# Performance work log

Hardware: AMD Instinct MI355X
Metric: run time of the kernel (lower is better)

## Reference

```python
import jax, jax.numpy as jnp
import numpy as np

B, T, D = 8, 2048, 512
S = 4                 # n_slots
SLOT_DIM = D          # cfg.slot_dim defaults to d_model
SE = 8                # state_embed_dim
GH = 64               # gate_hidden
EMA = 0.99
SIGMA_FLOOR = 1e-3
OPEN2CLOSING, CLOSING2LOCKED, UNLOCK = 0.1, 0.03, 0.25
GAINS = jnp.array([1.0, 0.5, 0.1], dtype=jnp.float32)  # OPEN, CLOSING, LOCKED


def _glorot(k, shape, fi, fo):
    b = (6.0 / (fi + fo)) ** 0.5
    return jax.random.uniform(k, shape, jnp.float32, -b, b)


def setup_inputs() -> dict:
    key = jax.random.key(0)
    ks = jax.random.split(key, 8)
    gate_in = D + 1 + SE  # [h, z, state_embed]
    return {
        'h_seq': jax.random.normal(ks[0], (B, T, D), jnp.float32),
        'pred_W': _glorot(ks[1], (S, D, D), D, D),
        'pred_b': jnp.zeros((S, D), jnp.float32),
        'gate_W1': _glorot(ks[2], (S, gate_in, GH), gate_in, GH),
        'gate_b1': jnp.zeros((S, GH), jnp.float32),
        'gate_W2': _glorot(ks[3], (S, GH, 1), GH, 1),
        'gate_b2': jnp.zeros((S, 1), jnp.float32),
        'write_W': _glorot(ks[4], (S, D, SLOT_DIM), D, SLOT_DIM),
        'write_b': jnp.zeros((S, SLOT_DIM), jnp.float32),
        'w0': jnp.zeros((S, SLOT_DIM), jnp.float32),
        'state_embed': jax.random.normal(ks[5], (3, SE), jnp.float32),
    }


def reference(h_seq, pred_W, pred_b, gate_W1, gate_b1, gate_W2, gate_b2,
              write_W, write_b, w0, state_embed):
    Bb, Tt, Dd = h_seq.shape
    h_det = jax.lax.stop_gradient(h_seq)
    # per-slot next-step predictions (input detached, as in torch): (B,T,S,D)
    preds = jnp.einsum('btd,sdo->btso', h_det, pred_W) + pred_b
    # prediction emitted at t-1 targets h_t
    pred_prev = jnp.concatenate([jnp.zeros_like(preds[:, :1]), preds[:, :-1]], axis=1)
    valid = jnp.arange(Tt) > 0  # no surprise signal at t=0

    m0 = jnp.broadcast_to(w0, (Bb, S, SLOT_DIM)).astype(h_seq.dtype)
    carry0 = (m0,
              jnp.zeros((S,), jnp.float32),       # mu
              jnp.ones((S,), jnp.float32),        # sigma
              jnp.full((S,), 0.5, jnp.float32),   # gate_ema
              jnp.zeros((S,), jnp.int32))         # slot_state

    def step(carry, xs):
        m, mu, sigma, gate_ema, state = carry
        h_t, p_prev, ok = xs  # (B,D), (B,S,D), scalar bool
        # prediction-error surprise per slot
        err = jnp.sqrt(jnp.sum((p_prev - h_t[:, None, :]) ** 2, axis=-1) + 1e-8)  # (B,S)
        err = jnp.where(ok, err, 0.0)
        z = (err - mu) / jnp.maximum(sigma, SIGMA_FLOOR)  # (B,S)
        # gate MLP over [h, z, state_embed]
        se = state_embed[state]  # (S,SE)
        gin = jnp.concatenate([
            jnp.broadcast_to(h_t[:, None, :], (Bb, S, Dd)),
            z[..., None],
            jnp.broadcast_to(se[None], (Bb, S, SE))], axis=-1)
        hid = jax.nn.relu(jnp.einsum('bsi,sih->bsh', gin, gate_W1) + gate_b1)
        g = jax.nn.sigmoid(jnp.einsum('bsh,sho->bso', hid, gate_W2) + gate_b2)[..., 0]  # (B,S)
        # state-dependent write gain (OPEN/CLOSING/LOCKED)
        g_eff = g * GAINS[state]
        w_enc = jnp.einsum('bd,sdo->bso', h_t, write_W) + write_b
        m = (1.0 - g_eff[..., None]) * m + g_eff[..., None] * w_enc
        read = m.reshape(Bb, S * SLOT_DIM)
        # homeostatic bookkeeping (buffers: non-differentiable, EMA)
        err_s = jax.lax.stop_gradient(err)
        mu_n = jnp.where(ok, EMA * mu + (1 - EMA) * err_s.mean(0), mu)
        sigma_n = jnp.where(ok, EMA * sigma + (1 - EMA) * jnp.abs(err_s - mu).mean(0), sigma)
        gate_ema_n = EMA * gate_ema + (1 - EMA) * jax.lax.stop_gradient(g).mean(0)
        # state machine transitions on gate EMA
        st = jnp.where((state == 0) & (gate_ema_n < OPEN2CLOSING), 1, state)
        st = jnp.where((state == 1) & (gate_ema_n < CLOSING2LOCKED), 2,
             jnp.where((state == 1) & (gate_ema_n > UNLOCK), 0, st))
        st = jnp.where((state == 2) & (gate_ema_n > UNLOCK), 0, st)
        return (m, mu_n, sigma_n, gate_ema_n, st), read

    xs = (jnp.swapaxes(h_seq, 0, 1), jnp.swapaxes(pred_prev, 0, 1), valid)
    _, reads = jax.lax.scan(step, carry0, xs)
    return jnp.swapaxes(reads, 0, 1)  # (B,T,S*SLOT_DIM)
```

## Files before the change

### kernel.cpp

```cpp
#include <hip/hip_runtime.h>
#include <hip/hip_bf16.h>

#define Bb 8
#define Tt 2048
#define Dd 512
#define Ss 4
#define GHh 64
#define NCHUNK 64
#define CH 32

typedef __hip_bfloat16 bf16;
typedef short bf16x8 __attribute__((ext_vector_type(8)));
typedef short bf16x4 __attribute__((ext_vector_type(4)));
typedef float f32x4 __attribute__((ext_vector_type(4)));
__device__ __forceinline__ float b2f(bf16 x){ return __bfloat162float(x); }
__device__ __forceinline__ float b2fs(short x){ bf16 t; __builtin_memcpy(&t,&x,2); return __bfloat162float(t); }

#define GLOAD_LDS16(g, l) \
  __builtin_amdgcn_global_load_lds((const __attribute__((address_space(1))) unsigned int*)(const void*)(g), \
                                   (__attribute__((address_space(3))) unsigned int*)(l), 16, 0, 0)

__global__ __launch_bounds__(256) void k0a_cvt(const float* __restrict__ h, bf16* __restrict__ hb){
  int i = (blockIdx.x*256 + threadIdx.x)*4;
  float4 v = *reinterpret_cast<const float4*>(&h[i]);
  hb[i+0] = __float2bfloat16(v.x);
  hb[i+1] = __float2bfloat16(v.y);
  hb[i+2] = __float2bfloat16(v.z);
  hb[i+3] = __float2bfloat16(v.w);
}

__global__ __launch_bounds__(256) void k0b_pack(const float* __restrict__ predW,
    const float* __restrict__ writeW, const float* __restrict__ gateW1, bf16* __restrict__ Wt){
  __shared__ float tile[32][33];
  int k0 = blockIdx.x*32, n0 = blockIdx.y*32;
  int tx = threadIdx.x & 31, ty = threadIdx.x >> 5;
  #pragma unroll
  for (int p = 0; p < 4; ++p) {
    int kk = ty + p*8;
    int n = n0 + tx, k = k0 + kk;
    float v;
    if (n < 2048)      { int s=n>>9, o=n&511;              v = predW[((size_t)s*512+k)*512+o]; }
    else if (n < 4096) { int n2=n-2048; int s=n2>>9,o=n2&511; v = writeW[((size_t)s*512+k)*512+o]; }
    else               { int n2=n-4096; int s=n2>>6,hh=n2&63; v = gateW1[((size_t)s*521+k)*64+hh]; }
    tile[kk][tx] = v;
  }
  __syncthreads();
  #pragma unroll
  for (int p = 0; p < 4; ++p) {
    int nn = ty + p*8;
    Wt[(size_t)(n0+nn)*512 + k0 + tx] = __float2bfloat16(tile[tx][nn]);
  }
}

__global__ __launch_bounds__(256) void k1_mfma(
    const bf16* __restrict__ hb, const bf16* __restrict__ Wt,
    const float* __restrict__ h, const float* __restrict__ predb, const float* __restrict__ writeb,
    bf16* __restrict__ wenc, float* __restrict__ hg, float* __restrict__ errsq)
{
  __shared__ bf16 As[2][128*64];
  __shared__ bf16 Bs[2][128*64];
  const int tid = threadIdx.x;
  const int w = tid >> 6, lane = tid & 63;
  const int bid = blockIdx.x;
  const int work = (bid & 7) * 544 + (bid >> 3);
  const int n0   = (work % 34) * 128;
  const int row0 = (work / 34) * 128;
  const int wm = w & 1, wn = w >> 1;
  const int mrow = lane & 15, kq = lane >> 4;

  f32x4 acc[4][4];
  #pragma unroll
  for (int i=0;i<4;++i)
    #pragma unroll
    for (int j=0;j<4;++j) acc[i][j] = (f32x4){0.f,0.f,0.f,0.f};

  const int srow  = lane >> 3;
  const int sslot = (lane & 7) ^ srow;
  const bf16* gaBase = hb + (size_t)(row0 + w*32 + srow)*512 + sslot*8;
  const bf16* gbBase = Wt + (size_t)(n0  + w*32 + srow)*512 + sslot*8;

  auto STAGE = [&](int buf, int kstep){
    const bf16* ga = gaBase + kstep*64;
    const bf16* gb = gbBase + kstep*64;
    bf16* lA = &As[buf][(w*32)*64];
    bf16* lB = &Bs[buf][(w*32)*64];
    #pragma unroll
    for (int i=0;i<4;++i) {
      GLOAD_LDS16(ga + (size_t)i*8*512, lA + i*8*64);
      GLOAD_LDS16(gb + (size_t)i*8*512, lB + i*8*64);
    }
  };

  auto COMPUTE = [&](int buf){
    #pragma unroll
    for (int kk=0; kk<2; ++kk) {
      bf16x8 af[4], bfr[4];
      #pragma unroll
      for (int mi=0;mi<4;++mi) {
        int r = wm*64 + mi*16 + mrow;
        af[mi] = *reinterpret_cast<const bf16x8*>(&As[buf][r*64 + (((kk*4+kq) ^ (r&7))<<3)]);
      }
      #pragma unroll
      for (int ni=0;ni<4;++ni) {
        int r = wn*64 + ni*16 + mrow;
        bfr[ni] = *reinterpret_cast<const bf16x8*>(&Bs[buf][r*64 + (((kk*4+kq) ^ (r&7))<<3)]);
      }
      #pragma unroll
      for (int mi=0;mi<4;++mi)
        #pragma unroll
        for (int ni=0;ni<4;++ni)
          acc[mi][ni] = __builtin_amdgcn_mfma_f32_16x16x32_bf16(af[mi], bfr[ni], acc[mi][ni], 0, 0, 0);
    }
  };

  STAGE(0, 0);
  __syncthreads();
  #pragma unroll
  for (int t = 0; t < 8; ++t) {
    if (t < 7) STAGE((t+1)&1, t+1);
    COMPUTE(t&1);
    __syncthreads();
  }

  if (n0 < 2048) {
    const int s = n0 >> 9;
    #pragma unroll
    for (int mi=0;mi<4;++mi) {
      #pragma unroll
      for (int reg=0;reg<4;++reg) {
        int r = row0 + wm*64 + mi*16 + kq*4 + reg;
        float sum = 0.f;
        if ((r & 2047) != 2047) {
          #pragma unroll
          for (int ni=0;ni<4;++ni) {
            int o = (n0 & 511) + wn*64 + ni*16 + mrow;
            float P = acc[mi][ni][reg] + predb[s*512 + o];
            float d = P - h[(size_t)(r+1)*512 + o];
            sum = fmaf(d, d, sum);
          }
        }
        #pragma unroll
        for (int off=1; off<16; off<<=1) sum += __shfl_xor(sum, off);
        if (mrow == 0 && (r & 2047) != 2047)
          atomicAdd(&errsq[(size_t)(r+1)*4 + s], sum);
      }
    }
  } else if (n0 < 4096) {
    #pragma unroll
    for (int mi=0;mi<4;++mi)
      #pragma unroll
      for (int ni=0;ni<4;++ni) {
        int n2 = n0 - 2048 + wn*64 + ni*16 + mrow;
        int s = n2 >> 9, o = n2 & 511;
        float wb = writeb[s*512 + o];
        #pragma unroll
        for (int reg=0;reg<4;++reg) {
          int r = row0 + wm*64 + mi*16 + kq*4 + reg;
          wenc[((size_t)r*4 + s)*512 + o] = __float2bfloat16(acc[mi][ni][reg] + wb);
        }
      }
  } else {
    #pragma unroll
    for (int mi=0;mi<4;++mi)
      #pragma unroll
      for (int ni=0;ni<4;++ni) {
        int n2 = n0 - 4096 + wn*64 + ni*16 + mrow;
        int s = n2 >> 6, hh = n2 & 63;
        #pragma unroll
        for (int reg=0;reg<4;++reg) {
          int r = row0 + wm*64 + mi*16 + kq*4 + reg;
          hg[((size_t)r*4 + s)*64 + hh] = acc[mi][ni][reg];
        }
      }
  }
}

__global__ void k2ab(const float* __restrict__ errsq, float* __restrict__ err, float* __restrict__ em){
  int i = blockIdx.x*256 + threadIdx.x;
  int t = i >> 2;
  float sum = 0.f;
  #pragma unroll
  for (int b=0;b<8;++b){
    float e = (t > 0) ? sqrtf(errsq[b*8192 + i] + 1e-8f) : 0.f;
    err[b*8192 + i] = e;
    sum += e;
  }
  em[i] = sum * 0.125f;
}

__global__ __launch_bounds__(256) void k2c_scan(const float* __restrict__ in, float* __restrict__ outv, float init){
  __shared__ float s_in[8192];
  __shared__ float sA[256], sB[256], s_entry[256];
  for (int i = threadIdx.x; i < 8192; i += 256) s_in[i] = in[i];
  __syncthreads();
  const int c = threadIdx.x >> 2, s = threadIdx.x & 3;
  float A = 1.f, B = 0.f;
  #pragma unroll 8
  for (int i = 0; i < 32; ++i) {
    int t = c*32 + i;
    if (t >= 1) { A *= 0.99f; B = fmaf(0.99f, B, 0.01f * s_in[t*4 + s]); }
  }
  sA[threadIdx.x] = A; sB[threadIdx.x] = B;
  __syncthreads();
  if (threadIdx.x < 4) {
    int ss = threadIdx.x;
    float v = init;
    for (int cc = 0; cc < 64; ++cc) {
      s_entry[cc*4 + ss] = v;
      v = fmaf(sA[cc*4 + ss], v, sB[cc*4 + ss]);
    }
  }
  __syncthreads();
  float v = s_entry[threadIdx.x];
  #pragma unroll 8
  for (int i = 0; i < 32; ++i) {
    int t = c*32 + i;
    outv[t*4 + s] = v;
    if (t >= 1) v = fmaf(0.99f, v, 0.01f * s_in[t*4 + s]);
  }
}

__global__ void k2d_sd(const float* __restrict__ err, const float* __restrict__ MU, float* __restrict__ sd){
  int i = blockIdx.x*256 + threadIdx.x;
  float mu = MU[i];
  float sum = 0.f;
  #pragma unroll
  for (int b=0;b<8;++b) sum += fabsf(err[b*8192 + i] - mu);
  sd[i] = sum * 0.125f;
}

__global__ void k2e_base(const float* __restrict__ gateW1, const float* __restrict__ semb,
                         const float* __restrict__ gateb1, float* __restrict__ base1){
  int i = blockIdx.x*256 + threadIdx.x;
  if (i < 768) {
    int hh = i & 63, k = (i >> 6) % 3, s = i / 192;
    float acc = gateb1[s*64 + hh];
    #pragma unroll
    for (int e = 0; e < 8; ++e)
      acc = fmaf(semb[k*8+e], gateW1[((size_t)s*521 + 513 + e)*64 + hh], acc);
    base1[i] = acc;
  }
}

__global__ void k3_gall(const float* __restrict__ hg, const float* __restrict__ err,
    const float* __restrict__ MU, const float* __restrict__ SIG,
    const float* __restrict__ gateW1, const float* __restrict__ base1,
    const float* __restrict__ gateW2, const float* __restrict__ gateb2,
    float* __restrict__ g_all)
{
  int i = blockIdx.x*256 + threadIdx.x;
  int k = i % 3;
  int bts = i / 3;
  int s = bts & 3;
  int t = (bts >> 2) & 2047;
  float e = err[bts];
  float z = (e - MU[t*4+s]) / fmaxf(SIG[t*4+s], 1e-3f);
  const float4* hgp  = reinterpret_cast<const float4*>(&hg[(size_t)bts*64]);
  const float4* b1p  = reinterpret_cast<const float4*>(&base1[(s*3 + k)*64]);
  const float4* w1zp = reinterpret_cast<const float4*>(&gateW1[((size_t)s*521 + 512)*64]);
  const float4* w2p  = reinterpret_cast<const float4*>(&gateW2[s*64]);
  float logit = 0.f;
  #pragma unroll
  for (int hq = 0; hq < 16; ++hq) {
    float4 hv = hgp[hq], bv = b1p[hq], wz = w1zp[hq], w2 = w2p[hq];
    logit = fmaf(fmaxf(fmaf(z, wz.x, hv.x) + bv.x, 0.f), w2.x, logit);
    logit = fmaf(fmaxf(fmaf(z, wz.y, hv.y) + bv.y, 0.f), w2.y, logit);
    logit = fmaf(fmaxf(fmaf(z, wz.z, hv.z) + bv.z, 0.f), w2.z, logit);
    logit = fmaf(fmaxf(fmaf(z, wz.w, hv.w) + bv.w, 0.f), w2.w, logit);
  }
  logit += gateb2[s];
  g_all[i] = 1.f/(1.f + expf(-logit));
}

__global__ void k3b_gm(const float* __restrict__ g_all, float* __restrict__ gm){
  int i = blockIdx.x*256 + threadIdx.x;
  float sum = 0.f;
  #pragma unroll
  for (int b=0;b<8;++b) sum += g_all[((size_t)b*8192 + i/3)*3 + (i%3)];
  gm[i] = sum * 0.125f;
}

__global__ __launch_bounds__(256) void k4_scan(const float* __restrict__ gm, int* __restrict__ states){
  __shared__ float s_gm[2][6144];
  for (int i = threadIdx.x; i < 6144; i += 256) s_gm[0][i] = gm[i];
  __syncthreads();
  float ema = 0.5f; int st = 0;
  for (int c = 0; c < 4; ++c) {
    if (c < 3)
      for (int i = threadIdx.x; i < 6144; i += 256) s_gm[(c+1)&1][i] = gm[(c+1)*6144 + i];
    if (threadIdx.x < 4) {
      int s = threadIdx.x;
      const float* gp = &s_gm[c&1][s*3];
      int* sp = &states[c*2048 + s];
      #pragma unroll 8
      for (int tt = 0; tt < 512; ++tt) {
        sp[tt*4] = st;
        float g0 = gp[tt*12+0], g1 = gp[tt*12+1], g2 = gp[tt*12+2];
        float base = 0.99f * ema;
        float e0 = fmaf(0.01f, g0, base);
        float e1 = fmaf(0.01f, g1, base);
        float e2 = fmaf(0.01f, g2, base);
        ema = (st == 0) ? e0 : ((st == 1) ? e1 : e2);
        int n0 = (ema < 0.1f) ? 1 : 0;
        int n1 = (ema < 0.03f) ? 2 : ((ema > 0.25f) ? 0 : 1);
        int n2 = (ema > 0.25f) ? 0 : 2;
        st = (st == 0) ? n0 : ((st == 1) ? n1 : n2);
      }
    }
    __syncthreads();
  }
}

__global__ void k5_a(const float* __restrict__ g_all, const int* __restrict__ states, float* __restrict__ a){
  int i = blockIdx.x*256 + threadIdx.x;
  int ts = i & 8191;
  int st = states[ts];
  float gain = (st == 0) ? 1.f : ((st == 1) ? 0.5f : 0.1f);
  a[i] = g_all[(size_t)i*3 + st] * gain;
}

__global__ __launch_bounds__(64) void k6_pass1(const float* __restrict__ a, const bf16* __restrict__ wenc,
      float* __restrict__ q, float* __restrict__ Pc){
  int c = blockIdx.x, s = blockIdx.y, b = blockIdx.z;
  int d0 = threadIdx.x * 4;
  __shared__ float s_a[CH];
  if (threadIdx.x < CH) s_a[threadIdx.x] = a[(size_t)(b*2048 + c*CH + threadIdx.x)*4 + s];
  __syncthreads();
  float qv[8];
  #pragma unroll
  for (int j=0;j<8;++j) qv[j] = 0.f;
  float p = 1.f;
  const bf16* wp = &wenc[((size_t)(b*2048 + c*CH)*4 + s)*512];
  #pragma unroll 4
  for (int i = 0; i < CH; ++i) {
    float av = s_a[i];
    float om = 1.f - av;
    bf16x4 w1 = *reinterpret_cast<const bf16x4*>(wp + (size_t)i*2048 + d0);
    bf16x4 w2 = *reinterpret_cast<const bf16x4*>(wp + (size_t)i*2048 + 256 + d0);
    #pragma unroll
    for (int j=0;j<4;++j) qv[j]   = fmaf(om, qv[j],   av*b2fs(w1[j]));
    #pragma unroll
    for (int j=0;j<4;++j) qv[4+j] = fmaf(om, qv[4+j], av*b2fs(w2[j]));
    p *= om;
  }
  float* qp = &q[((size_t)(b*4+s)*NCHUNK + c)*512];
  *reinterpret_cast<float4*>(qp + d0)       = make_float4(qv[0],qv[1],qv[2],qv[3]);
  *reinterpret_cast<float4*>(qp + 256 + d0) = make_float4(qv[4],qv[5],qv[6],qv[7]);
  if (threadIdx.x == 0) Pc[(b*4+s)*NCHUNK + c] = p;
}

__global__ __launch_bounds__(128) void k7_bound(const float* __restrict__ q, const float* __restrict__ Pc,
      const float* __restrict__ w0, float* __restrict__ m_start){
  int s = blockIdx.x, b = blockIdx.y, d4 = threadIdx.x * 4;
  float4 m = *reinterpret_cast<const float4*>(&w0[s*512 + d4]);
  for (int c = 0; c < NCHUNK; ++c) {
    *reinterpret_cast<float4*>(&m_start[((size_t)(b*4+s)*NCHUNK + c)*512 + d4]) = m;
    float pc = Pc[(b*4+s)*NCHUNK + c];
    float4 qv = *reinterpret_cast<const float4*>(&q[((size_t)(b*4+s)*NCHUNK + c)*512 + d4]);
    m.x = fmaf(pc, m.x, qv.x);
    m.y = fmaf(pc, m.y, qv.y);
    m.z = fmaf(pc, m.z, qv.z);
    m.w = fmaf(pc, m.w, qv.w);
  }
}

__global__ __launch_bounds__(64) void k8_pass2(const float* __restrict__ a, const bf16* __restrict__ wenc,
      const float* __restrict__ m_start, float* __restrict__ out){
  int c = blockIdx.x, s = blockIdx.y, b = blockIdx.z;
  int d0 = threadIdx.x * 4;
  __shared__ float s_a[CH];
  if (threadIdx.x < CH) s_a[threadIdx.x] = a[(size_t)(b*2048 + c*CH + threadIdx.x)*4 + s];
  __syncthreads();
  const float* msp = &m_start[((size_t)(b*4+s)*NCHUNK + c)*512];
  float4 m1 = *reinterpret_cast<const float4*>(msp + d0);
  float4 m2 = *reinterpret_cast<const float4*>(msp + 256 + d0);
  const bf16* wp = &wenc[((size_t)(b*2048 + c*CH)*4 + s)*512];
  float* op = &out[((size_t)(b*2048 + c*CH))*2048 + s*512];
  #pragma unroll 2
  for (int i = 0; i < CH; ++i) {
    float av = s_a[i];
    float om = 1.f - av;
    bf16x4 w1 = *reinterpret_cast<const bf16x4*>(wp + (size_t)i*2048 + d0);
    bf16x4 w2 = *reinterpret_cast<const bf16x4*>(wp + (size_t)i*2048 + 256 + d0);
    m1.x = fmaf(om, m1.x, av*b2fs(w1[0]));
    m1.y = fmaf(om, m1.y, av*b2fs(w1[1]));
    m1.z = fmaf(om, m1.z, av*b2fs(w1[2]));
    m1.w = fmaf(om, m1.w, av*b2fs(w1[3]));
    m2.x = fmaf(om, m2.x, av*b2fs(w2[0]));
    m2.y = fmaf(om, m2.y, av*b2fs(w2[1]));
    m2.z = fmaf(om, m2.z, av*b2fs(w2[2]));
    m2.w = fmaf(om, m2.w, av*b2fs(w2[3]));
    *reinterpret_cast<float4*>(op + (size_t)i*2048 + d0)       = m1;
    *reinterpret_cast<float4*>(op + (size_t)i*2048 + 256 + d0) = m2;
  }
}

extern "C" void kernel_launch(void* const* d_in, const int* in_sizes, int n_in,
                              void* d_out, int out_size, void* d_ws, size_t ws_size,
                              hipStream_t stream) {
  (void)in_sizes; (void)n_in; (void)out_size; (void)ws_size;
  const float* h      = (const float*)d_in[0];
  const float* predW  = (const float*)d_in[1];
  const float* predb  = (const float*)d_in[2];
  const float* gateW1 = (const float*)d_in[3];
  const float* gateb1 = (const float*)d_in[4];
  const float* gateW2 = (const float*)d_in[5];
  const float* gateb2 = (const float*)d_in[6];
  const float* writeW = (const float*)d_in[7];
  const float* writeb = (const float*)d_in[8];
  const float* w0     = (const float*)d_in[9];
  const float* semb   = (const float*)d_in[10];
  float* out = (float*)d_out;

  char* ws = (char*)d_ws;
  size_t off = 0;
  auto alloc = [&](size_t bytes) -> char* {
    char* p = ws + off; off += (bytes + 255) / 256 * 256; return p;
  };
  bf16*  wenc   = (bf16*) alloc((size_t)Bb*Tt*Ss*Dd*2);
  float* hg     = (float*)alloc((size_t)Bb*Tt*Ss*GHh*4);
  bf16*  hb     = (bf16*) alloc((size_t)Bb*Tt*Dd*2);
  bf16*  Wt     = (bf16*) alloc((size_t)4352*512*2);
  float* errsq  = (float*)alloc((size_t)Bb*Tt*Ss*4);
  float* err    = (float*)alloc((size_t)Bb*Tt*Ss*4);
  float* em     = (float*)alloc((size_t)Tt*Ss*4);
  float* MU     = (float*)alloc((size_t)Tt*Ss*4);
  float* sd     = (float*)alloc((size_t)Tt*Ss*4);
  float* SIG    = (float*)alloc((size_t)Tt*Ss*4);
  float* base1  = (float*)alloc((size_t)Ss*3*GHh*4);
  float* g_all  = (float*)alloc((size_t)Bb*Tt*Ss*3*4);
  float* gm     = (float*)alloc((size_t)Tt*Ss*3*4);
  int*   states = (int*)  alloc((size_t)Tt*Ss*4);
  float* av     = (float*)alloc((size_t)Bb*Tt*Ss*4);
  float* Pc     = (float*)alloc((size_t)Bb*Ss*NCHUNK*4);
  float* q      = (float*)alloc((size_t)Bb*Ss*NCHUNK*Dd*4);
  float* mst    = (float*)alloc((size_t)Bb*Ss*NCHUNK*Dd*4);

  hipMemsetAsync(errsq, 0, (size_t)Bb*Tt*Ss*4, stream);

  k0a_cvt<<<(Bb*Tt*Dd)/(256*4), 256, 0, stream>>>(h, hb);
  dim3 g0b(16, 136);
  k0b_pack<<<g0b, 256, 0, stream>>>(predW, writeW, gateW1, Wt);
  k1_mfma<<<4352, 256, 0, stream>>>(hb, Wt, h, predb, writeb, wenc, hg, errsq);
  k2ab<<<(Tt*Ss)/256, 256, 0, stream>>>(errsq, err, em);
  k2c_scan<<<1, 256, 0, stream>>>(em, MU, 0.f);
  k2d_sd<<<(Tt*Ss)/256, 256, 0, stream>>>(err, MU, sd);
  k2c_scan<<<1, 256, 0, stream>>>(sd, SIG, 1.f);
  k2e_base<<<3, 256, 0, stream>>>(gateW1, semb, gateb1, base1);
  k3_gall<<<(Bb*Tt*Ss*3)/256, 256, 0, stream>>>(hg, err, MU, SIG, gateW1, base1, gateW2, gateb2, g_all);
  k3b_gm<<<(Tt*Ss*3)/256, 256, 0, stream>>>(g_all, gm);
  k4_scan<<<1, 256, 0, stream>>>(gm, states);
  k5_a<<<(Bb*Tt*Ss)/256, 256, 0, stream>>>(g_all, states, av);
  dim3 g6(NCHUNK, Ss, Bb);
  k6_pass1<<<g6, 64, 0, stream>>>(av, wenc, q, Pc);
  dim3 g7(Ss, Bb);
  k7_bound<<<g7, 128, 0, stream>>>(q, Pc, w0, mst);
  k8_pass2<<<g6, 64, 0, stream>>>(av, wenc, mst, out);
}
```

Before: 619.0 us.

## Enlarge GEMM tiles to 256x256 and fuse error statistics kernels into one

The fused projection GEMM moves from 128x128 tiles with 256 threads to 256x256 tiles with 512 threads on a 2D grid. This doubles operand reuse per LDS load and drops the XCD-aware block swizzle. Separately, the five small kernels that compute error norms, the two EMA scans and the gate base terms are merged into one single-block kernel, keeping intermediates in shared memory and saving launches. The trade-offs are larger LDS and register use with fewer, coarser blocks (a possible tail effect), and the error reduction now runs serially in one block instead of across many.

```diff
diff --git a/kernel.cpp b/kernel.cpp
--- a/kernel.cpp
+++ b/kernel.cpp
@@ -52,25 +52,23 @@
   }
 }
 
-__global__ __launch_bounds__(256) void k1_mfma(
+__global__ __launch_bounds__(512) void k1_mfma(
     const bf16* __restrict__ hb, const bf16* __restrict__ Wt,
     const float* __restrict__ h, const float* __restrict__ predb, const float* __restrict__ writeb,
     bf16* __restrict__ wenc, float* __restrict__ hg, float* __restrict__ errsq)
 {
-  __shared__ bf16 As[2][128*64];
-  __shared__ bf16 Bs[2][128*64];
+  __shared__ bf16 As[2][256*64];
+  __shared__ bf16 Bs[2][256*64];
   const int tid = threadIdx.x;
   const int w = tid >> 6, lane = tid & 63;
-  const int bid = blockIdx.x;
-  const int work = (bid & 7) * 544 + (bid >> 3);
-  const int n0   = (work % 34) * 128;
-  const int row0 = (work / 34) * 128;
+  const int n0 = blockIdx.x * 256;
+  const int row0 = blockIdx.y * 256;
   const int wm = w & 1, wn = w >> 1;
   const int mrow = lane & 15, kq = lane >> 4;
 
-  f32x4 acc[4][4];
-  #pragma unroll
-  for (int i=0;i<4;++i)
+  f32x4 acc[8][4];
+  #pragma unroll
+  for (int i=0;i<8;++i)
     #pragma unroll
     for (int j=0;j<4;++j) acc[i][j] = (f32x4){0.f,0.f,0.f,0.f};
 
@@ -94,22 +92,20 @@
   auto COMPUTE = [&](int buf){
     #pragma unroll
     for (int kk=0; kk<2; ++kk) {
-      bf16x8 af[4], bfr[4];
-      #pragma unroll
-      for (int mi=0;mi<4;++mi) {
-        int r = wm*64 + mi*16 + mrow;
-        af[mi] = *reinterpret_cast<const bf16x8*>(&As[buf][r*64 + (((kk*4+kq) ^ (r&7))<<3)]);
-      }
+      bf16x8 bfr[4];
       #pragma unroll
       for (int ni=0;ni<4;++ni) {
         int r = wn*64 + ni*16 + mrow;
         bfr[ni] = *reinterpret_cast<const bf16x8*>(&Bs[buf][r*64 + (((kk*4+kq) ^ (r&7))<<3)]);
       }
       #pragma unroll
-      for (int mi=0;mi<4;++mi)
+      for (int mi=0;mi<8;++mi) {
+        int r = wm*128 + mi*16 + mrow;
+        bf16x8 af = *reinterpret_cast<const bf16x8*>(&As[buf][r*64 + (((kk*4+kq) ^ (r&7))<<3)]);
         #pragma unroll
         for (int ni=0;ni<4;++ni)
-          acc[mi][ni] = __builtin_amdgcn_mfma_f32_16x16x32_bf16(af[mi], bfr[ni], acc[mi][ni], 0, 0, 0);
+          acc[mi][ni] = __builtin_amdgcn_mfma_f32_16x16x32_bf16(af, bfr[ni], acc[mi][ni], 0, 0, 0);
+      }
     }
   };
 
@@ -125,10 +121,10 @@
   if (n0 < 2048) {
     const int s = n0 >> 9;
     #pragma unroll
-    for (int mi=0;mi<4;++mi) {
+    for (int mi=0;mi<8;++mi) {
       #pragma unroll
       for (int reg=0;reg<4;++reg) {
-        int r = row0 + wm*64 + mi*16 + kq*4 + reg;
+        int r = row0 + wm*128 + mi*16 + kq*4 + reg;
         float sum = 0.f;
         if ((r & 2047) != 2047) {
           #pragma unroll
@@ -147,7 +143,7 @@
     }
   } else if (n0 < 4096) {
     #pragma unroll
-    for (int mi=0;mi<4;++mi)
+    for (int mi=0;mi<8;++mi)
       #pragma unroll
       for (int ni=0;ni<4;++ni) {
         int n2 = n0 - 2048 + wn*64 + ni*16 + mrow;
@@ -155,84 +151,101 @@
         float wb = writeb[s*512 + o];
         #pragma unroll
         for (int reg=0;reg<4;++reg) {
-          int r = row0 + wm*64 + mi*16 + kq*4 + reg;
+          int r = row0 + wm*128 + mi*16 + kq*4 + reg;
           wenc[((size_t)r*4 + s)*512 + o] = __float2bfloat16(acc[mi][ni][reg] + wb);
         }
       }
   } else {
     #pragma unroll
-    for (int mi=0;mi<4;++mi)
+    for (int mi=0;mi<8;++mi)
       #pragma unroll
       for (int ni=0;ni<4;++ni) {
-        int n2 = n0 - 4096 + wn*64 + ni*16 + mrow;
+        int n2 = wn*64 + ni*16 + mrow;
         int s = n2 >> 6, hh = n2 & 63;
         #pragma unroll
         for (int reg=0;reg<4;++reg) {
-          int r = row0 + wm*64 + mi*16 + kq*4 + reg;
+          int r = row0 + wm*128 + mi*16 + kq*4 + reg;
           hg[((size_t)r*4 + s)*64 + hh] = acc[mi][ni][reg];
         }
       }
   }
 }
 
-__global__ void k2ab(const float* __restrict__ errsq, float* __restrict__ err, float* __restrict__ em){
-  int i = blockIdx.x*256 + threadIdx.x;
-  int t = i >> 2;
-  float sum = 0.f;
-  #pragma unroll
-  for (int b=0;b<8;++b){
-    float e = (t > 0) ? sqrtf(errsq[b*8192 + i] + 1e-8f) : 0.f;
-    err[b*8192 + i] = e;
-    sum += e;
-  }
-  em[i] = sum * 0.125f;
-}
-
-__global__ __launch_bounds__(256) void k2c_scan(const float* __restrict__ in, float* __restrict__ outv, float init){
-  __shared__ float s_in[8192];
+__global__ __launch_bounds__(256) void k2_fused(const float* __restrict__ errsq,
+    const float* __restrict__ gateW1, const float* __restrict__ semb, const float* __restrict__ gateb1,
+    float* __restrict__ err, float* __restrict__ MU, float* __restrict__ SIG, float* __restrict__ base1){
+  __shared__ float s_em[8192];
+  __shared__ float s_mu[8192];
   __shared__ float sA[256], sB[256], s_entry[256];
-  for (int i = threadIdx.x; i < 8192; i += 256) s_in[i] = in[i];
-  __syncthreads();
-  const int c = threadIdx.x >> 2, s = threadIdx.x & 3;
-  float A = 1.f, B = 0.f;
-  #pragma unroll 8
-  for (int i = 0; i < 32; ++i) {
-    int t = c*32 + i;
-    if (t >= 1) { A *= 0.99f; B = fmaf(0.99f, B, 0.01f * s_in[t*4 + s]); }
-  }
-  sA[threadIdx.x] = A; sB[threadIdx.x] = B;
-  __syncthreads();
-  if (threadIdx.x < 4) {
-    int ss = threadIdx.x;
-    float v = init;
-    for (int cc = 0; cc < 64; ++cc) {
-      s_entry[cc*4 + ss] = v;
-      v = fmaf(sA[cc*4 + ss], v, sB[cc*4 + ss]);
-    }
-  }
-  __syncthreads();
-  float v = s_entry[threadIdx.x];
-  #pragma unroll 8
-  for (int i = 0; i < 32; ++i) {
-    int t = c*32 + i;
-    outv[t*4 + s] = v;
-    if (t >= 1) v = fmaf(0.99f, v, 0.01f * s_in[t*4 + s]);
-  }
-}
-
-__global__ void k2d_sd(const float* __restrict__ err, const float* __restrict__ MU, float* __restrict__ sd){
-  int i = blockIdx.x*256 + threadIdx.x;
-  float mu = MU[i];
-  float sum = 0.f;
-  #pragma unroll
-  for (int b=0;b<8;++b) sum += fabsf(err[b*8192 + i] - mu);
-  sd[i] = sum * 0.125f;
-}
-
-__global__ void k2e_base(const float* __restrict__ gateW1, const float* __restrict__ semb,
-                         const float* __restrict__ gateb1, float* __restrict__ base1){
-  int i = blockIdx.x*256 + threadIdx.x;
-  if (i < 768) {
+  const int tid = threadIdx.x;
+  for (int i = tid; i < 8192; i += 256) {
+    int t = i >> 2;
+    float sum = 0.f;
+    #pragma unroll
+    for (int b=0;b<8;++b){
+      float e = (t > 0) ? sqrtf(errsq[b*8192 + i] + 1e-8f) : 0.f;
+      err[b*8192 + i] = e;
+      sum += e;
+    }
+    s_em[i] = sum * 0.125f;
+  }
+  __syncthreads();
+  {
+    const int c = tid >> 2, s = tid & 3;
+    float A = 1.f, Bv = 0.f;
+    #pragma unroll 8
+    for (int i2 = 0; i2 < 32; ++i2) {
+      int t = c*32 + i2;
+      if (t >= 1) { A *= 0.99f; Bv = fmaf(0.99f, Bv, 0.01f * s_em[t*4 + s]); }
+    }
+    sA[tid] = A; sB[tid] = Bv;
+    __syncthreads();
+    if (tid < 4) {
+      float v = 0.f;
+      for (int cc = 0; cc < 64; ++cc) { s_entry[cc*4 + tid] = v; v = fmaf(sA[cc*4 + tid], v, sB[cc*4 + tid]); }
+    }
+    __syncthreads();
+    float v = s_entry[tid];
+    #pragma unroll 8
+    for (int i2 = 0; i2 < 32; ++i2) {
+      int t = c*32 + i2;
+      s_mu[t*4 + s] = v; MU[t*4 + s] = v;
+      if (t >= 1) v = fmaf(0.99f, v, 0.01f * s_em[t*4 + s]);
+    }
+  }
+  __syncthreads();
+  for (int i = tid; i < 8192; i += 256) {
+    float mu = s_mu[i];
+    float sum = 0.f;
+    #pragma unroll
+    for (int b=0;b<8;++b) sum += fabsf(err[b*8192 + i] - mu);
+    s_em[i] = sum * 0.125f;
+  }
+  __syncthreads();
+  {
+    const int c = tid >> 2, s = tid & 3;
+    float A = 1.f, Bv = 0.f;
+    #pragma unroll 8
+    for (int i2 = 0; i2 < 32; ++i2) {
+      int t = c*32 + i2;
+      if (t >= 1) { A *= 0.99f; Bv = fmaf(0.99f, Bv, 0.01f * s_em[t*4 + s]); }
+    }
+    sA[tid] = A; sB[tid] = Bv;
+    __syncthreads();
+    if (tid < 4) {
+      float v = 1.f;
+      for (int cc = 0; cc < 64; ++cc) { s_entry[cc*4 + tid] = v; v = fmaf(sA[cc*4 + tid], v, sB[cc*4 + tid]); }
+    }
+    __syncthreads();
+    float v = s_entry[tid];
+    #pragma unroll 8
+    for (int i2 = 0; i2 < 32; ++i2) {
+      int t = c*32 + i2;
+      SIG[t*4 + s] = v;
+      if (t >= 1) v = fmaf(0.99f, v, 0.01f * s_em[t*4 + s]);
+    }
+  }
+  for (int i = tid; i < 768; i += 256) {
     int hh = i & 63, k = (i >> 6) % 3, s = i / 192;
     float acc = gateb1[s*64 + hh];
     #pragma unroll
@@ -423,9 +436,7 @@
   bf16*  Wt     = (bf16*) alloc((size_t)4352*512*2);
   float* errsq  = (float*)alloc((size_t)Bb*Tt*Ss*4);
   float* err    = (float*)alloc((size_t)Bb*Tt*Ss*4);
-  float* em     = (float*)alloc((size_t)Tt*Ss*4);
   float* MU     = (float*)alloc((size_t)Tt*Ss*4);
-  float* sd     = (float*)alloc((size_t)Tt*Ss*4);
   float* SIG    = (float*)alloc((size_t)Tt*Ss*4);
   float* base1  = (float*)alloc((size_t)Ss*3*GHh*4);
   float* g_all  = (float*)alloc((size_t)Bb*Tt*Ss*3*4);
@@ -441,12 +452,9 @@
   k0a_cvt<<<(Bb*Tt*Dd)/(256*4), 256, 0, stream>>>(h, hb);
   dim3 g0b(16, 136);
   k0b_pack<<<g0b, 256, 0, stream>>>(predW, writeW, gateW1, Wt);
-  k1_mfma<<<4352, 256, 0, stream>>>(hb, Wt, h, predb, writeb, wenc, hg, errsq);
-  k2ab<<<(Tt*Ss)/256, 256, 0, stream>>>(errsq, err, em);
-  k2c_scan<<<1, 256, 0, stream>>>(em, MU, 0.f);
-  k2d_sd<<<(Tt*Ss)/256, 256, 0, stream>>>(err, MU, sd);
-  k2c_scan<<<1, 256, 0, stream>>>(sd, SIG, 1.f);
-  k2e_base<<<3, 256, 0, stream>>>(gateW1, semb, gateb1, base1);
+  dim3 g1(17, 64);
+  k1_mfma<<<g1, 512, 0, stream>>>(hb, Wt, h, predb, writeb, wenc, hg, errsq);
+  k2_fused<<<1, 256, 0, stream>>>(errsq, gateW1, semb, gateb1, err, MU, SIG, base1);
   k3_gall<<<(Bb*Tt*Ss*3)/256, 256, 0, stream>>>(hg, err, MU, SIG, gateW1, base1, gateW2, gateb2, g_all);
   k3b_gm<<<(Tt*Ss*3)/256, 256, 0, stream>>>(g_all, gm);
   k4_scan<<<1, 256, 0, stream>>>(gm, states);
```

Result: no change. 631.2 us (+2.0%).

## Enlarge MFMA GEMM tile to 256x256, share gate logits, fuse gain kernel

Applied to the files above, without the earlier changes.

The projection GEMM moves from 128x128 tiles with 256 threads to 256x256 tiles with 512 threads (8 waves), doubling per-wave M work to raise operand reuse from LDS. The swizzled block-order remap is replaced by a plain 2D grid. The gate kernel now computes all three state logits per thread, reusing the hidden and z loads. The separate k5 gain/select kernel is folded into the chunk scan kernels, which removes one launch and the av buffer. Risks: 128 KB of LDS per block, which lowers occupancy; a 128-register accumulator that could cause spills; and a grid of only 1088 blocks, which may balance poorly across CUs and L2.

```diff
diff --git a/kernel.cpp b/kernel.cpp
--- a/kernel.cpp
+++ b/kernel.cpp
@@ -52,25 +52,23 @@
   }
 }
 
-__global__ __launch_bounds__(256) void k1_mfma(
+__global__ __launch_bounds__(512) void k1_mfma(
     const bf16* __restrict__ hb, const bf16* __restrict__ Wt,
     const float* __restrict__ h, const float* __restrict__ predb, const float* __restrict__ writeb,
     bf16* __restrict__ wenc, float* __restrict__ hg, float* __restrict__ errsq)
 {
-  __shared__ bf16 As[2][128*64];
-  __shared__ bf16 Bs[2][128*64];
+  __shared__ bf16 As[2][256*64];
+  __shared__ bf16 Bs[2][256*64];
   const int tid = threadIdx.x;
   const int w = tid >> 6, lane = tid & 63;
-  const int bid = blockIdx.x;
-  const int work = (bid & 7) * 544 + (bid >> 3);
-  const int n0   = (work % 34) * 128;
-  const int row0 = (work / 34) * 128;
+  const int n0 = blockIdx.x * 256;
+  const int row0 = blockIdx.y * 256;
   const int wm = w & 1, wn = w >> 1;
   const int mrow = lane & 15, kq = lane >> 4;
 
-  f32x4 acc[4][4];
-  #pragma unroll
-  for (int i=0;i<4;++i)
+  f32x4 acc[8][4];
+  #pragma unroll
+  for (int i=0;i<8;++i)
     #pragma unroll
     for (int j=0;j<4;++j) acc[i][j] = (f32x4){0.f,0.f,0.f,0.f};
 
@@ -94,22 +92,20 @@
   auto COMPUTE = [&](int buf){
     #pragma unroll
     for (int kk=0; kk<2; ++kk) {
-      bf16x8 af[4], bfr[4];
-      #pragma unroll
-      for (int mi=0;mi<4;++mi) {
-        int r = wm*64 + mi*16 + mrow;
-        af[mi] = *reinterpret_cast<const bf16x8*>(&As[buf][r*64 + (((kk*4+kq) ^ (r&7))<<3)]);
-      }
+      bf16x8 bfr[4];
       #pragma unroll
       for (int ni=0;ni<4;++ni) {
         int r = wn*64 + ni*16 + mrow;
         bfr[ni] = *reinterpret_cast<const bf16x8*>(&Bs[buf][r*64 + (((kk*4+kq) ^ (r&7))<<3)]);
       }
       #pragma unroll
-      for (int mi=0;mi<4;++mi)
+      for (int mi=0;mi<8;++mi) {
+        int r = wm*128 + mi*16 + mrow;
+        bf16x8 af = *reinterpret_cast<const bf16x8*>(&As[buf][r*64 + (((kk*4+kq) ^ (r&7))<<3)]);
         #pragma unroll
         for (int ni=0;ni<4;++ni)
-          acc[mi][ni] = __builtin_amdgcn_mfma_f32_16x16x32_bf16(af[mi], bfr[ni], acc[mi][ni], 0, 0, 0);
+          acc[mi][ni] = __builtin_amdgcn_mfma_f32_16x16x32_bf16(af, bfr[ni], acc[mi][ni], 0, 0, 0);
+      }
     }
   };
 
@@ -125,10 +121,10 @@
   if (n0 < 2048) {
     const int s = n0 >> 9;
     #pragma unroll
-    for (int mi=0;mi<4;++mi) {
+    for (int mi=0;mi<8;++mi) {
       #pragma unroll
       for (int reg=0;reg<4;++reg) {
-        int r = row0 + wm*64 + mi*16 + kq*4 + reg;
+        int r = row0 + wm*128 + mi*16 + kq*4 + reg;
         float sum = 0.f;
         if ((r & 2047) != 2047) {
           #pragma unroll
@@ -147,7 +143,7 @@
     }
   } else if (n0 < 4096) {
     #pragma unroll
-    for (int mi=0;mi<4;++mi)
+    for (int mi=0;mi<8;++mi)
       #pragma unroll
       for (int ni=0;ni<4;++ni) {
         int n2 = n0 - 2048 + wn*64 + ni*16 + mrow;
@@ -155,20 +151,20 @@
         float wb = writeb[s*512 + o];
         #pragma unroll
         for (int reg=0;reg<4;++reg) {
-          int r = row0 + wm*64 + mi*16 + kq*4 + reg;
+          int r = row0 + wm*128 + mi*16 + kq*4 + reg;
           wenc[((size_t)r*4 + s)*512 + o] = __float2bfloat16(acc[mi][ni][reg] + wb);
         }
       }
   } else {
     #pragma unroll
-    for (int mi=0;mi<4;++mi)
+    for (int mi=0;mi<8;++mi)
       #pragma unroll
       for (int ni=0;ni<4;++ni) {
-        int n2 = n0 - 4096 + wn*64 + ni*16 + mrow;
+        int n2 = wn*64 + ni*16 + mrow;
         int s = n2 >> 6, hh = n2 & 63;
         #pragma unroll
         for (int reg=0;reg<4;++reg) {
-          int r = row0 + wm*64 + mi*16 + kq*4 + reg;
+          int r = row0 + wm*128 + mi*16 + kq*4 + reg;
           hg[((size_t)r*4 + s)*64 + hh] = acc[mi][ni][reg];
         }
       }
@@ -242,34 +238,47 @@
   }
 }
 
-__global__ void k3_gall(const float* __restrict__ hg, const float* __restrict__ err,
+__global__ __launch_bounds__(256) void k3_gall(const float* __restrict__ hg, const float* __restrict__ err,
     const float* __restrict__ MU, const float* __restrict__ SIG,
     const float* __restrict__ gateW1, const float* __restrict__ base1,
     const float* __restrict__ gateW2, const float* __restrict__ gateb2,
     float* __restrict__ g_all)
 {
-  int i = blockIdx.x*256 + threadIdx.x;
-  int k = i % 3;
-  int bts = i / 3;
+  int bts = blockIdx.x*256 + threadIdx.x;
   int s = bts & 3;
   int t = (bts >> 2) & 2047;
   float e = err[bts];
   float z = (e - MU[t*4+s]) / fmaxf(SIG[t*4+s], 1e-3f);
   const float4* hgp  = reinterpret_cast<const float4*>(&hg[(size_t)bts*64]);
-  const float4* b1p  = reinterpret_cast<const float4*>(&base1[(s*3 + k)*64]);
   const float4* w1zp = reinterpret_cast<const float4*>(&gateW1[((size_t)s*521 + 512)*64]);
   const float4* w2p  = reinterpret_cast<const float4*>(&gateW2[s*64]);
-  float logit = 0.f;
+  const float4* b0p  = reinterpret_cast<const float4*>(&base1[(s*3 + 0)*64]);
+  const float4* b1p  = reinterpret_cast<const float4*>(&base1[(s*3 + 1)*64]);
+  const float4* b2p  = reinterpret_cast<const float4*>(&base1[(s*3 + 2)*64]);
+  float l0 = 0.f, l1 = 0.f, l2 = 0.f;
   #pragma unroll
   for (int hq = 0; hq < 16; ++hq) {
-    float4 hv = hgp[hq], bv = b1p[hq], wz = w1zp[hq], w2 = w2p[hq];
-    logit = fmaf(fmaxf(fmaf(z, wz.x, hv.x) + bv.x, 0.f), w2.x, logit);
-    logit = fmaf(fmaxf(fmaf(z, wz.y, hv.y) + bv.y, 0.f), w2.y, logit);
-    logit = fmaf(fmaxf(fmaf(z, wz.z, hv.z) + bv.z, 0.f), w2.z, logit);
-    logit = fmaf(fmaxf(fmaf(z, wz.w, hv.w) + bv.w, 0.f), w2.w, logit);
-  }
-  logit += gateb2[s];
-  g_all[i] = 1.f/(1.f + expf(-logit));
+    float4 hv = hgp[hq], wz = w1zp[hq], w2 = w2p[hq];
+    float4 b0 = b0p[hq], b1 = b1p[hq], b2 = b2p[hq];
+    float cx = fmaf(z, wz.x, hv.x), cy = fmaf(z, wz.y, hv.y);
+    float cz = fmaf(z, wz.z, hv.z), cw = fmaf(z, wz.w, hv.w);
+    l0 = fmaf(fmaxf(cx + b0.x, 0.f), w2.x, l0);
+    l0 = fmaf(fmaxf(cy + b0.y, 0.f), w2.y, l0);
+    l0 = fmaf(fmaxf(cz + b0.z, 0.f), w2.z, l0);
+    l0 = fmaf(fmaxf(cw + b0.w, 0.f), w2.w, l0);
+    l1 = fmaf(fmaxf(cx + b1.x, 0.f), w2.x, l1);
+    l1 = fmaf(fmaxf(cy + b1.y, 0.f), w2.y, l1);
+    l1 = fmaf(fmaxf(cz + b1.z, 0.f), w2.z, l1);
+    l1 = fmaf(fmaxf(cw + b1.w, 0.f), w2.w, l1);
+    l2 = fmaf(fmaxf(cx + b2.x, 0.f), w2.x, l2);
+    l2 = fmaf(fmaxf(cy + b2.y, 0.f), w2.y, l2);
+    l2 = fmaf(fmaxf(cz + b2.z, 0.f), w2.z, l2);
+    l2 = fmaf(fmaxf(cw + b2.w, 0.f), w2.w, l2);
+  }
+  float gb = gateb2[s];
+  g_all[(size_t)bts*3 + 0] = 1.f/(1.f + expf(-(l0 + gb)));
+  g_all[(size_t)bts*3 + 1] = 1.f/(1.f + expf(-(l1 + gb)));
+  g_all[(size_t)bts*3 + 2] = 1.f/(1.f + expf(-(l2 + gb)));
 }
 
 __global__ void k3b_gm(const float* __restrict__ g_all, float* __restrict__ gm){
@@ -311,20 +320,17 @@
   }
 }
 
-__global__ void k5_a(const float* __restrict__ g_all, const int* __restrict__ states, float* __restrict__ a){
-  int i = blockIdx.x*256 + threadIdx.x;
-  int ts = i & 8191;
-  int st = states[ts];
-  float gain = (st == 0) ? 1.f : ((st == 1) ? 0.5f : 0.1f);
-  a[i] = g_all[(size_t)i*3 + st] * gain;
-}
-
-__global__ __launch_bounds__(64) void k6_pass1(const float* __restrict__ a, const bf16* __restrict__ wenc,
-      float* __restrict__ q, float* __restrict__ Pc){
+__global__ __launch_bounds__(64) void k6_pass1(const float* __restrict__ g_all, const int* __restrict__ states,
+      const bf16* __restrict__ wenc, float* __restrict__ q, float* __restrict__ Pc){
   int c = blockIdx.x, s = blockIdx.y, b = blockIdx.z;
   int d0 = threadIdx.x * 4;
   __shared__ float s_a[CH];
-  if (threadIdx.x < CH) s_a[threadIdx.x] = a[(size_t)(b*2048 + c*CH + threadIdx.x)*4 + s];
+  if (threadIdx.x < CH) {
+    int t = c*CH + threadIdx.x;
+    int st = states[t*4 + s];
+    float gain = (st == 0) ? 1.f : ((st == 1) ? 0.5f : 0.1f);
+    s_a[threadIdx.x] = g_all[((size_t)(b*2048 + t)*4 + s)*3 + st] * gain;
+  }
   __syncthreads();
   float qv[8];
   #pragma unroll
@@ -364,12 +370,17 @@
   }
 }
 
-__global__ __launch_bounds__(64) void k8_pass2(const float* __restrict__ a, const bf16* __restrict__ wenc,
-      const float* __restrict__ m_start, float* __restrict__ out){
+__global__ __launch_bounds__(64) void k8_pass2(const float* __restrict__ g_all, const int* __restrict__ states,
+      const bf16* __restrict__ wenc, const float* __restrict__ m_start, float* __restrict__ out){
   int c = blockIdx.x, s = blockIdx.y, b = blockIdx.z;
   int d0 = threadIdx.x * 4;
   __shared__ float s_a[CH];
-  if (threadIdx.x < CH) s_a[threadIdx.x] = a[(size_t)(b*2048 + c*CH + threadIdx.x)*4 + s];
+  if (threadIdx.x < CH) {
+    int t = c*CH + threadIdx.x;
+    int st = states[t*4 + s];
+    float gain = (st == 0) ? 1.f : ((st == 1) ? 0.5f : 0.1f);
+    s_a[threadIdx.x] = g_all[((size_t)(b*2048 + t)*4 + s)*3 + st] * gain;
+  }
   __syncthreads();
   const float* msp = &m_start[((size_t)(b*4+s)*NCHUNK + c)*512];
   float4 m1 = *reinterpret_cast<const float4*>(msp + d0);
@@ -431,7 +442,6 @@
   float* g_all  = (float*)alloc((size_t)Bb*Tt*Ss*3*4);
   float* gm     = (float*)alloc((size_t)Tt*Ss*3*4);
   int*   states = (int*)  alloc((size_t)Tt*Ss*4);
-  float* av     = (float*)alloc((size_t)Bb*Tt*Ss*4);
   float* Pc     = (float*)alloc((size_t)Bb*Ss*NCHUNK*4);
   float* q      = (float*)alloc((size_t)Bb*Ss*NCHUNK*Dd*4);
   float* mst    = (float*)alloc((size_t)Bb*Ss*NCHUNK*Dd*4);
@@ -441,19 +451,19 @@
   k0a_cvt<<<(Bb*Tt*Dd)/(256*4), 256, 0, stream>>>(h, hb);
   dim3 g0b(16, 136);
   k0b_pack<<<g0b, 256, 0, stream>>>(predW, writeW, gateW1, Wt);
-  k1_mfma<<<4352, 256, 0, stream>>>(hb, Wt, h, predb, writeb, wenc, hg, errsq);
+  dim3 g1(17, 64);
+  k1_mfma<<<g1, 512, 0, stream>>>(hb, Wt, h, predb, writeb, wenc, hg, errsq);
   k2ab<<<(Tt*Ss)/256, 256, 0, stream>>>(errsq, err, em);
   k2c_scan<<<1, 256, 0, stream>>>(em, MU, 0.f);
   k2d_sd<<<(Tt*Ss)/256, 256, 0, stream>>>(err, MU, sd);
   k2c_scan<<<1, 256, 0, stream>>>(sd, SIG, 1.f);
   k2e_base<<<3, 256, 0, stream>>>(gateW1, semb, gateb1, base1);
-  k3_gall<<<(Bb*Tt*Ss*3)/256, 256, 0, stream>>>(hg, err, MU, SIG, gateW1, base1, gateW2, gateb2, g_all);
+  k3_gall<<<(Bb*Tt*Ss)/256, 256, 0, stream>>>(hg, err, MU, SIG, gateW1, base1, gateW2, gateb2, g_all);
   k3b_gm<<<(Tt*Ss*3)/256, 256, 0, stream>>>(g_all, gm);
   k4_scan<<<1, 256, 0, stream>>>(gm, states);
-  k5_a<<<(Bb*Tt*Ss)/256, 256, 0, stream>>>(g_all, states, av);
   dim3 g6(NCHUNK, Ss, Bb);
-  k6_pass1<<<g6, 64, 0, stream>>>(av, wenc, q, Pc);
+  k6_pass1<<<g6, 64, 0, stream>>>(g_all, states, wenc, q, Pc);
   dim3 g7(Ss, Bb);
   k7_bound<<<g7, 128, 0, stream>>>(q, Pc, w0, mst);
-  k8_pass2<<<g6, 64, 0, stream>>>(av, wenc, mst, out);
-}
+  k8_pass2<<<g6, 64, 0, stream>>>(g_all, states, wenc, mst, out);
+}
```

New measurement: 542.1 us. 1.14x faster.
